# Kernel tuning notes

Measured on AMD Instinct MI355X. Metric: run time of the kernel, lower is better.

The kernel has to match this reference:

```python
import jax, jax.numpy as jnp
import numpy as np

EPS = 1e-8

def unit_projection(x):
    # project each embedding vector so its Fourier coefficients have unit magnitude
    f = jnp.fft.fft(x, axis=-1)
    f = f / jnp.maximum(jnp.abs(f), EPS)
    return jnp.real(jnp.fft.ifft(f, axis=-1))

def bind(a, b):
    return jnp.fft.irfft(jnp.fft.rfft(a, axis=-1) * jnp.fft.rfft(b, axis=-1), n=a.shape[-1], axis=-1)

def unbind(s, k):
    # k is unit-magnitude in Fourier domain, so its inverse is its conjugate
    return jnp.fft.irfft(jnp.fft.rfft(s, axis=-1) * jnp.conj(jnp.fft.rfft(k, axis=-1)), n=s.shape[-1], axis=-1)

def layer_norm(x, g, b):
    mu = jnp.mean(x, axis=-1, keepdims=True)
    var = jnp.var(x, axis=-1, keepdims=True)
    return (x - mu) * jax.lax.rsqrt(var + 1e-5) * g + b

def setup_inputs():
    key = jax.random.key(0)
    ks = jax.random.split(key, 12)
    B, S, D = 4, 2048, 1024
    sc = 1.0 / np.sqrt(D)
    inp = {
        'x': jax.random.normal(ks[0], (B, S, D), jnp.float32),
        'Wq': jax.random.normal(ks[1], (D, D), jnp.float32) * sc,
        'bq': jnp.zeros((D,), jnp.float32),
        'Wk': jax.random.normal(ks[2], (D, D), jnp.float32) * sc,
        'bk': jnp.zeros((D,), jnp.float32),
        'Wv': jax.random.normal(ks[3], (D, D), jnp.float32) * sc,
        'bv': jnp.zeros((D,), jnp.float32),
        'ln1_g': jnp.ones((D,), jnp.float32), 'ln1_b': jnp.zeros((D,), jnp.float32),
        'ln2_g': jnp.ones((D,), jnp.float32), 'ln2_b': jnp.zeros((D,), jnp.float32),
        'W1': jax.random.normal(ks[4], (D, 4 * D), jnp.float32) * sc,
        'b1': jnp.zeros((4 * D,), jnp.float32),
        'W2': jax.random.normal(ks[5], (4 * D, D), jnp.float32) * (1.0 / np.sqrt(4 * D)),
        'b2': jnp.zeros((D,), jnp.float32),
    }
    return inp

def reference(x, Wq, bq, Wk, bk, Wv, bv, ln1_g, ln1_b, ln2_g, ln2_b, W1, b1, W2, b2):
    h = layer_norm(x, ln1_g, ln1_b)
    q = unit_projection(h @ Wq + bq)
    k = unit_projection(h @ Wk + bk)
    v = unit_projection(h @ Wv + bv)
    s = jnp.cumsum(bind(k, v), axis=1)  # causal prefix-sum over sequence
    mixed = unbind(s, q)
    x = x + mixed  # dropout=0.0
    h2 = layer_norm(x, ln2_g, ln2_b)
    mlp = jax.nn.gelu(h2 @ W1 + b1, approximate=False) @ W2 + b2
    return x + mlp
```

## Files before the change

### kernel.cpp

```cpp
#include <hip/hip_runtime.h>
#include <cstdint>
#include <cstddef>

#define DD 1024
#define SSEQ 2048
#define NB 4
#define MROWS 8192
#define FBINS 513
#define FPAD 520
#define WFP 1152
#define NQKV 3456
#define NHID 4096
#define NCHUNK 64
#define SCHUNK 32

typedef _Float16 f16_t;
typedef _Float16 f16x8 __attribute__((ext_vector_type(8)));
typedef _Float16 f16x2 __attribute__((ext_vector_type(2)));
typedef float f32x4 __attribute__((ext_vector_type(4)));

__device__ __forceinline__ float2 cmul(float2 a, float2 b) {
  return make_float2(a.x * b.x - a.y * b.y, a.x * b.y + a.y * b.x);
}

__device__ __forceinline__ void async_cp16(const void* g, void* l) {
  __builtin_amdgcn_global_load_lds(
      (const __attribute__((address_space(1))) void*)g,
      (__attribute__((address_space(3))) void*)l, 16, 0, 0);
}

template <int N> __device__ __forceinline__ void vwait();
template <> __device__ __forceinline__ void vwait<0>() { asm volatile("s_waitcnt vmcnt(0)" ::: "memory"); }
template <> __device__ __forceinline__ void vwait<1>() { asm volatile("s_waitcnt vmcnt(1)" ::: "memory"); }
template <> __device__ __forceinline__ void vwait<2>() { asm volatile("s_waitcnt vmcnt(2)" ::: "memory"); }
template <> __device__ __forceinline__ void vwait<3>() { asm volatile("s_waitcnt vmcnt(3)" ::: "memory"); }
template <> __device__ __forceinline__ void vwait<4>() { asm volatile("s_waitcnt vmcnt(4)" ::: "memory"); }

__device__ __forceinline__ float fast_gelu(float val) {
  float av = __builtin_fabsf(val);
  float z = av * 0.70710678118654752f;
  float t = __builtin_amdgcn_rcpf(__builtin_fmaf(0.3275911f, z, 1.0f));
  float poly = t * __builtin_fmaf(t,
      __builtin_fmaf(t, __builtin_fmaf(t,
          __builtin_fmaf(t, 1.061405429f, -1.453152027f),
          1.421413741f), -0.284496736f), 0.254829592f);
  float e = __builtin_amdgcn_exp2f(z * z * -1.4426950408889634f);
  float w = poly * e;
  float r = fmaxf(val, 0.0f);
  return __builtin_fmaf(-0.5f * av, w, r);
}

__device__ __forceinline__ void fft1024(float2* bufA, float2* bufB,
                                        const float2* tw, int tid) {
  float2* s = bufA;
  float2* d = bufB;
  for (int m = 1; m < 1024; m <<= 1) {
#pragma unroll
    for (int r2 = 0; r2 < 2; ++r2) {
      int u = tid + r2 * 256;
      int k = u & (m - 1);
      int jm = u - k;
      float2 c0 = s[u];
      float2 c1 = s[u + 512];
      float2 wt = tw[jm];
      float2 su = make_float2(c0.x + c1.x, c0.y + c1.y);
      float2 df = make_float2(c0.x - c1.x, c0.y - c1.y);
      float2 pr = cmul(wt, df);
      d[2 * jm + k] = su;
      d[2 * jm + k + m] = pr;
    }
    __syncthreads();
    float2* tmp = s; s = d; d = tmp;
  }
}

__device__ __forceinline__ float2* fft512(float2* bufA, float2* bufB,
                                          const float2* tw, int tid) {
  float2* s = bufA;
  float2* d = bufB;
  for (int m = 1; m < 512; m <<= 1) {
    int u = tid;
    int k = u & (m - 1);
    int jm = u - k;
    float2 c0 = s[u];
    float2 c1 = s[u + 256];
    float2 wt = tw[jm];
    float2 su = make_float2(c0.x + c1.x, c0.y + c1.y);
    float2 df = make_float2(c0.x - c1.x, c0.y - c1.y);
    float2 pr = cmul(wt, df);
    d[2 * jm + k] = su;
    d[2 * jm + k + m] = pr;
    __syncthreads();
    float2* tmp = s; s = d; d = tmp;
  }
  return s;
}

__global__ __launch_bounds__(256) void wfft_k(
    const float* __restrict__ Wq, const float* __restrict__ Wk,
    const float* __restrict__ Wv, float* __restrict__ WfAll) {
  __shared__ float2 tw[512];
  __shared__ float2 bufA[1024];
  __shared__ float2 bufB[1024];
  const int tid = threadIdx.x;
  const int p = blockIdx.x >> 10, k = blockIdx.x & 1023;
  const float* W = (p == 0) ? Wq : ((p == 1) ? Wk : Wv);
  for (int t = tid; t < 512; t += 256) {
    float ang = -6.2831853071795864769f * (float)t * (1.0f / 1024.0f);
    tw[t] = make_float2(cosf(ang), sinf(ang));
  }
  const float* src = W + (size_t)k * DD;
  for (int t = tid; t < 1024; t += 256) bufA[t] = make_float2(src[t], 0.f);
  __syncthreads();
  fft1024(bufA, bufB, tw, tid);
  float* dst = WfAll + ((size_t)p * DD + k) * WFP;
  for (int t = tid; t <= 512; t += 256) {
    float2 f = bufA[t];
    dst[2 * t] = f.x;
    dst[2 * t + 1] = f.y;
  }
  for (int j = 1026 + tid; j < WFP; j += 256) dst[j] = 0.f;
}

__global__ __launch_bounds__(256) void bfft_k(
    const float* __restrict__ bq, const float* __restrict__ bk,
    const float* __restrict__ bv, float* __restrict__ biasC) {
  __shared__ float2 tw[512];
  __shared__ float2 bufA[1024];
  __shared__ float2 bufB[1024];
  const int tid = threadIdx.x;
  const int p = blockIdx.x;
  const float* bsrc = (p == 0) ? bq : ((p == 1) ? bk : bv);
  for (int t = tid; t < 512; t += 256) {
    float ang = -6.2831853071795864769f * (float)t * (1.0f / 1024.0f);
    tw[t] = make_float2(cosf(ang), sinf(ang));
  }
  for (int t = tid; t < 1024; t += 256) bufA[t] = make_float2(bsrc[t], 0.f);
  __syncthreads();
  fft1024(bufA, bufB, tw, tid);
  float* dst = biasC + (size_t)p * WFP;
  for (int t = tid; t <= 512; t += 256) {
    float2 f = bufA[t];
    dst[2 * t] = f.x;
    dst[2 * t + 1] = f.y;
  }
  for (int j = 1026 + tid; j < WFP; j += 256) dst[j] = 0.f;
}

__global__ __launch_bounds__(256) void transpose_cast_k(
    const float* __restrict__ W, f16_t* __restrict__ Wt, int K, int N) {
  __shared__ float tile[32][33];
  const int tx = threadIdx.x & 31, ty = threadIdx.x >> 5;
  const int n0 = blockIdx.x * 32, k0 = blockIdx.y * 32;
#pragma unroll
  for (int i = 0; i < 32; i += 8)
    tile[ty + i][tx] = W[(size_t)(k0 + ty + i) * N + n0 + tx];
  __syncthreads();
#pragma unroll
  for (int i = 0; i < 32; i += 8)
    Wt[(size_t)(n0 + ty + i) * K + k0 + tx] = (f16_t)tile[tx][ty + i];
}

__global__ __launch_bounds__(256) void transpose_cast2_k(
    const float* __restrict__ W, f16_t* __restrict__ WtH,
    f16_t* __restrict__ WtL, int K, int N) {
  __shared__ float tile[32][33];
  const int tx = threadIdx.x & 31, ty = threadIdx.x >> 5;
  const int n0 = blockIdx.x * 32, k0 = blockIdx.y * 32;
#pragma unroll
  for (int i = 0; i < 32; i += 8)
    tile[ty + i][tx] = W[(size_t)(k0 + ty + i) * N + n0 + tx];
  __syncthreads();
#pragma unroll
  for (int i = 0; i < 32; i += 8) {
    float val = tile[tx][ty + i];
    f16_t hi = (f16_t)val;
    f16_t lo = (f16_t)(val - (float)hi);
    size_t idx = (size_t)(n0 + ty + i) * K + k0 + tx;
    WtH[idx] = hi;
    WtL[idx] = lo;
  }
}

__global__ __launch_bounds__(256) void ln_cast2_k(
    const float* __restrict__ x, const float* __restrict__ g,
    const float* __restrict__ b, f16_t* __restrict__ hH,
    f16_t* __restrict__ hL) {
  const int row = blockIdx.x, tid = threadIdx.x;
  __shared__ float red[8];
  const float* xr = x + (size_t)row * DD;
  float v[4], ls = 0.f, lq = 0.f;
#pragma unroll
  for (int i = 0; i < 4; ++i) {
    v[i] = xr[i * 256 + tid];
    ls += v[i];
    lq += v[i] * v[i];
  }
#pragma unroll
  for (int o = 32; o > 0; o >>= 1) {
    ls += __shfl_down(ls, o);
    lq += __shfl_down(lq, o);
  }
  const int lane = tid & 63, w = tid >> 6;
  if (lane == 0) { red[w] = ls; red[w + 4] = lq; }
  __syncthreads();
  const float S = red[0] + red[1] + red[2] + red[3];
  const float Q = red[4] + red[5] + red[6] + red[7];
  const float mean = S * (1.f / 1024.f);
  const float var = Q * (1.f / 1024.f) - mean * mean;
  const float rs = rsqrtf(var + 1e-5f);
#pragma unroll
  for (int i = 0; i < 4; ++i) {
    int n = i * 256 + tid;
    float val = (v[i] - mean) * rs * g[n] + b[n];
    f16_t hi = (f16_t)val;
    hH[(size_t)row * DD + n] = hi;
    hL[(size_t)row * DD + n] = (f16_t)(val - (float)hi);
  }
}

__global__ __launch_bounds__(256, 2) void gemm_qkv_k(
    const f16_t* __restrict__ Ahi, const f16_t* __restrict__ Alo,
    const f16_t* __restrict__ Bhi, const float* __restrict__ bias,
    float* __restrict__ outF) {
  __shared__ alignas(16) f16_t AsH[128 * 64];
  __shared__ alignas(16) f16_t AsL[128 * 64];
  __shared__ alignas(16) f16_t BsH[128 * 64];
  const int tid = threadIdx.x;
  const int lane = tid & 63;
  const int w = tid >> 6;
  const int wm = w >> 1, wn = w & 1;

  const int lin = blockIdx.x;
  const int s = (lin & 7) * 216 + (lin >> 3);
  const int g = s / 108;
  const int r = s % 108;
  const int n = r >> 2;
  const int m0 = g * 4 + (r & 3);
  const int bn = n * 128;
  const int bm = m0 * 128;
  const bool qmode = (n < 9);

  f32x4 acc[4][4];
#pragma unroll
  for (int i = 0; i < 4; ++i)
#pragma unroll
    for (int j = 0; j < 4; ++j) acc[i][j] = (f32x4){0.f, 0.f, 0.f, 0.f};

  const int srow = lane >> 3;
  const int slot = lane & 7;

  for (int kt = 0; kt < 1024; kt += 64) {
#pragma unroll
    for (int i = 0; i < 4; ++i) {
      const int rb = (i * 4 + w) * 8;
      const int row = rb + srow;
      const int gg = (slot - (row & 7)) & 7;
      size_t ga = (size_t)(bm + row) * 1024 + kt + gg * 8;
      size_t gb = (size_t)(bn + row) * 1024 + kt + gg * 8;
      async_cp16(Ahi + ga, &AsH[rb * 64]);
      if (qmode) async_cp16(Alo + ga, &AsL[rb * 64]);
      async_cp16(Bhi + gb, &BsH[rb * 64]);
    }
    __syncthreads();
#pragma unroll
    for (int ks = 0; ks < 2; ++ks) {
      const int cgbase = ks * 4 + (lane >> 4);
      f16x8 ah[4], bh[4];
#pragma unroll
      for (int mt = 0; mt < 4; ++mt) {
        int m = wm * 64 + mt * 16 + (lane & 15);
        int sl = (cgbase + (m & 7)) & 7;
        ah[mt] = *(const f16x8*)(&AsH[m * 64 + sl * 8]);
      }
#pragma unroll
      for (int nt = 0; nt < 4; ++nt) {
        int nn = wn * 64 + nt * 16 + (lane & 15);
        int sl = (cgbase + (nn & 7)) & 7;
        bh[nt] = *(const f16x8*)(&BsH[nn * 64 + sl * 8]);
      }
#pragma unroll
      for (int mt = 0; mt < 4; ++mt)
#pragma unroll
        for (int nt = 0; nt < 4; ++nt)
          acc[mt][nt] = __builtin_amdgcn_mfma_f32_16x16x32_f16(
              ah[mt], bh[nt], acc[mt][nt], 0, 0, 0);
      if (qmode) {
        f16x8 al[4];
#pragma unroll
        for (int mt = 0; mt < 4; ++mt) {
          int m = wm * 64 + mt * 16 + (lane & 15);
          int sl = (cgbase + (m & 7)) & 7;
          al[mt] = *(const f16x8*)(&AsL[m * 64 + sl * 8]);
        }
#pragma unroll
        for (int mt = 0; mt < 4; ++mt)
#pragma unroll
          for (int nt = 0; nt < 4; ++nt)
            acc[mt][nt] = __builtin_amdgcn_mfma_f32_16x16x32_f16(
                al[mt], bh[nt], acc[mt][nt], 0, 0, 0);
      }
    }
    __syncthreads();
  }

  const int q = lane >> 4;
  const int cn = lane & 15;
#pragma unroll
  for (int mt = 0; mt < 4; ++mt) {
#pragma unroll
    for (int nt = 0; nt < 4; ++nt) {
      const int gcol = bn + wn * 64 + nt * 16 + cn;
      const float bv = bias[gcol];
      const int grow0 = bm + wm * 64 + mt * 16 + q * 4;
#pragma unroll
      for (int i = 0; i < 4; ++i) {
        size_t idx = (size_t)(grow0 + i) * NQKV + gcol;
        outF[idx] = acc[mt][nt][i] + bv;
      }
    }
  }
}

template <int RHALF>
__device__ __forceinline__ void stage_half(const f16_t* __restrict__ G,
                                           int grow0, int ldk, int kt,
                                           f16_t* ls, int w, int lane) {
  const int srow = lane >> 3;
  const int slot = lane & 7;
#pragma unroll
  for (int j = 0; j < RHALF / 64; ++j) {
    const int rb = (w + j * 8) * 8;
    const int row = rb + srow;
    const int gg = (slot - (row & 7)) & 7;
    async_cp16(G + (size_t)(grow0 + row) * ldk + kt + gg * 8, ls + rb * 64);
  }
}

template <int BM, int BN>
__device__ __forceinline__ void readA(const f16_t* As, int mq, int wm, int lane,
                                      f16x8 (&aR)[BM / 64][2]) {
#pragma unroll
  for (int mf = 0; mf < BM / 64; ++mf) {
    const int m = mq * (BM / 2) + wm * (BM / 4) + mf * 16 + (lane & 15);
#pragma unroll
    for (int ks = 0; ks < 2; ++ks) {
      const int cg = ks * 4 + (lane >> 4);
      const int sl = (cg + (m & 7)) & 7;
      aR[mf][ks] = *(const f16x8*)(As + m * 64 + sl * 8);
    }
  }
}

template <int BM, int BN>
__device__ __forceinline__ void readB(const f16_t* Bs, int nq, int wn, int lane,
                                      f16x8 (&bR)[BN / 128][2]) {
#pragma unroll
  for (int nf = 0; nf < BN / 128; ++nf) {
    const int n = nq * (BN / 2) + wn * (BN / 8) + nf * 16 + (lane & 15);
#pragma unroll
    for (int ks = 0; ks < 2; ++ks) {
      const int cg = ks * 4 + (lane >> 4);
      const int sl = (cg + (n & 7)) & 7;
      bR[nf][ks] = *(const f16x8*)(Bs + n * 64 + sl * 8);
    }
  }
}

template <int MF, int NF>
__device__ __forceinline__ void mfma_q(f32x4 (&acc)[MF][NF],
                                       const f16x8 (&aR)[MF][2],
                                       const f16x8 (&bR)[NF][2]) {
#pragma unroll
  for (int ks = 0; ks < 2; ++ks)
#pragma unroll
    for (int mf = 0; mf < MF; ++mf)
#pragma unroll
      for (int nf = 0; nf < NF; ++nf)
        acc[mf][nf] = __builtin_amdgcn_mfma_f32_16x16x32_f16(
            aR[mf][ks], bR[nf][ks], acc[mf][nf], 0, 0, 0);
}

template <int BM, int BN, int MM, int NN, int KK, int EPI>
__global__ __launch_bounds__(512, 2) void gemm8p_k(
    const f16_t* __restrict__ A, const f16_t* __restrict__ Bt,
    const float* __restrict__ bias, const float* __restrict__ resid,
    float* __restrict__ outF, f16_t* __restrict__ outH) {
  constexpr int MF = BM / 64;
  constexpr int NF = BN / 128;
  constexpr int LA = BM / 128;
  constexpr int LB = BN / 128;
  constexpr int NT = KK / 64;
  constexpr int TILE = (BM + BN) * 64;
  __shared__ alignas(16) f16_t lds[2 * TILE];

  const int tid = threadIdx.x;
  const int lane = tid & 63;
  const int w = tid >> 6;
  const int wm = w >> 2;
  const int wn = w & 3;

  constexpr int ntm = MM / BM, ntn = NN / BN;
  constexpr int per = (ntm * ntn) / 8;
  const int lin = (int)blockIdx.x;
  const int s = (lin & 7) * per + (lin >> 3);
  const int bn = (s % ntn) * BN;
  const int bm = (s / ntn) * BM;

  f32x4 acc[2][2][MF][NF];
#pragma unroll
  for (int a0 = 0; a0 < 2; ++a0)
#pragma unroll
    for (int a1 = 0; a1 < 2; ++a1)
#pragma unroll
      for (int mf = 0; mf < MF; ++mf)
#pragma unroll
        for (int nf = 0; nf < NF; ++nf)
          acc[a0][a1][mf][nf] = (f32x4){0.f, 0.f, 0.f, 0.f};

  {
    f16_t* A0s = lds;
    f16_t* B0s = lds + BM * 64;
    stage_half<BM / 2>(A, bm, KK, 0, A0s, w, lane);
    stage_half<BN / 2>(Bt, bn, KK, 0, B0s, w, lane);
    stage_half<BN / 2>(Bt, bn + BN / 2, KK, 0, B0s + (BN / 2) * 64, w, lane);
    stage_half<BM / 2>(A, bm + BM / 2, KK, 0, A0s + (BM / 2) * 64, w, lane);
  }
  vwait<LA + LB>();
  __builtin_amdgcn_s_barrier();

  f16x8 aR[MF][2], bR0[NF][2], bR1[NF][2];

  for (int t = 0; t < NT; ++t) {
    const int cur = t & 1;
    f16_t* As = lds + cur * TILE;
    f16_t* Bs = As + BM * 64;
    f16_t* Asn = lds + (cur ^ 1) * TILE;
    f16_t* Bsn = Asn + BM * 64;
    const bool pre = (t + 1 < NT);
    const int ktn = (t + 1) << 6;

    readA<BM, BN>(As, 0, wm, lane, aR);
    readB<BM, BN>(Bs, 0, wn, lane, bR0);
    if (pre) stage_half<BM / 2>(A, bm, KK, ktn, Asn, w, lane);
    __builtin_amdgcn_s_barrier();
    __builtin_amdgcn_s_setprio(1);
    mfma_q<MF, NF>(acc[0][0], aR, bR0);
    __builtin_amdgcn_s_setprio(0);
    if (pre) vwait<2 * LA>(); else vwait<LA>();
    __builtin_amdgcn_s_barrier();

    readB<BM, BN>(Bs, 1, wn, lane, bR1);
    if (pre) stage_half<BN / 2>(Bt, bn, KK, ktn, Bsn, w, lane);
    __builtin_amdgcn_s_barrier();
    __builtin_amdgcn_s_setprio(1);
    mfma_q<MF, NF>(acc[0][1], aR, bR1);
    __builtin_amdgcn_s_setprio(0);
    if (pre) vwait<LA + LB>(); else vwait<0>();
    __builtin_amdgcn_s_barrier();

    readA<BM, BN>(As, 1, wm, lane, aR);
    if (pre) stage_half<BN / 2>(Bt, bn + BN / 2, KK, ktn,
                                Bsn + (BN / 2) * 64, w, lane);
    __builtin_amdgcn_s_barrier();
    __builtin_amdgcn_s_setprio(1);
    mfma_q<MF, NF>(acc[1][0], aR, bR0);
    __builtin_amdgcn_s_setprio(0);
    __builtin_amdgcn_s_barrier();

    if (pre) stage_half<BM / 2>(A, bm + BM / 2, KK, ktn,
                                Asn + (BM / 2) * 64, w, lane);
    __builtin_amdgcn_s_barrier();
    __builtin_amdgcn_s_setprio(1);
    mfma_q<MF, NF>(acc[1][1], aR, bR1);
    __builtin_amdgcn_s_setprio(0);
    if (pre) vwait<LA + LB>();
    __builtin_amdgcn_s_barrier();
  }

  const int q4 = lane >> 4;
  const int cn = lane & 15;
#pragma unroll
  for (int mq = 0; mq < 2; ++mq)
#pragma unroll
    for (int nq = 0; nq < 2; ++nq)
#pragma unroll
      for (int mf = 0; mf < MF; ++mf)
#pragma unroll
        for (int nf = 0; nf < NF; ++nf) {
          const int gcol = bn + nq * (BN / 2) + wn * (BN / 8) + nf * 16 + cn;
          const float bv = bias[gcol];
          const int grow0 = bm + mq * (BM / 2) + wm * (BM / 4) + mf * 16 + q4 * 4;
#pragma unroll
          for (int i = 0; i < 4; ++i) {
            const float val = acc[mq][nq][mf][nf][i] + bv;
            const size_t idx = (size_t)(grow0 + i) * NN + gcol;
            if (EPI == 1) {
              outH[idx] = (f16_t)fast_gelu(val);
            } else {
              outF[idx] = val + resid[idx];
            }
          }
        }
}

__device__ __forceinline__ float2 unitc(float2 a) {
  float inv = 1.0f / fmaxf(sqrtf(a.x * a.x + a.y * a.y), 1e-8f);
  return make_float2(a.x * inv, a.y * inv);
}
__device__ __forceinline__ float2 bind_bin(const float2* r, int f) {
  float2 kn = unitc(r[576 + f]);
  float2 vn = unitc(r[1152 + f]);
  return cmul(kn, vn);
}

__global__ __launch_bounds__(256) void scan_pass1_k(
    const float* __restrict__ qkvF, float2* __restrict__ T) {
  const int bid = blockIdx.x;
  const int sc = bid & 63;
  const int fh = (bid >> 6) & 1;
  const int b = bid >> 7;
  const int s0 = sc * SCHUNK;
  const float2* base = (const float2*)(qkvF + ((size_t)(b * SSEQ + s0)) * NQKV);
  for (int f = fh * 256 + threadIdx.x; f < FBINS; f += 512) {
    float2 acc = make_float2(0.f, 0.f);
    const float2* r = base;
    for (int i = 0; i < SCHUNK; ++i) {
      float2 pv = bind_bin(r, f);
      acc.x += pv.x; acc.y += pv.y;
      r += NQKV / 2;
    }
    T[((size_t)b * NCHUNK + sc) * FBINS + f] = acc;
  }
}

__global__ void scan_pass2_k(float2* __restrict__ T) {
  const int idx = blockIdx.x * 256 + threadIdx.x;
  if (idx >= NB * FBINS) return;
  const int b = idx / FBINS, f = idx % FBINS;
  float2 acc = make_float2(0.f, 0.f);
  for (int sc = 0; sc < NCHUNK; ++sc) {
    size_t a = ((size_t)b * NCHUNK + sc) * FBINS + f;
    float2 v = T[a];
    T[a] = acc;
    acc.x += v.x; acc.y += v.y;
  }
}

__global__ __launch_bounds__(256) void scan_pass3_k(
    const float* __restrict__ qkvF, const float2* __restrict__ T,
    float2* __restrict__ Scum) {
  const int bid = blockIdx.x;
  const int sc = bid & 63;
  const int fh = (bid >> 6) & 1;
  const int b = bid >> 7;
  const int s0 = sc * SCHUNK;
  const float2* base = (const float2*)(qkvF + ((size_t)(b * SSEQ + s0)) * NQKV);
  for (int f = fh * 256 + threadIdx.x; f < FBINS; f += 512) {
    float2 acc = T[((size_t)b * NCHUNK + sc) * FBINS + f];
    const float2* r = base;
    size_t orow = ((size_t)(b * SSEQ + s0)) * FPAD + f;
    for (int i = 0; i < SCHUNK; ++i) {
      float2 pv = bind_bin(r, f);
      acc.x += pv.x; acc.y += pv.y;
      Scum[orow] = acc;
      r += NQKV / 2;
      orow += FPAD;
    }
  }
}

__global__ __launch_bounds__(256) void unbind_ln2_k(
    const float2* __restrict__ Scum, const float* __restrict__ qkvF,
    const float* __restrict__ x, float* __restrict__ x2out,
    f16_t* __restrict__ h2, const float* __restrict__ g2,
    const float* __restrict__ b2) {
  __shared__ float2 tw[256];
  __shared__ float2 Marr[513];
  __shared__ float2 bufA[512];
  __shared__ float2 bufB[512];
  __shared__ float red[8];
  const int tid = threadIdx.x;
  const int row = blockIdx.x;

  {
    float ang = 6.2831853071795864769f * (float)tid * (1.0f / 512.0f);
    tw[tid] = make_float2(cosf(ang), sinf(ang));
  }
  const float2* qrow = (const float2*)(qkvF + (size_t)row * NQKV);
  for (int t = tid; t <= 512; t += 256) {
    float2 sc = Scum[(size_t)row * FPAD + t];
    float2 fq = unitc(qrow[t]);
    Marr[t] = make_float2(sc.x * fq.x + sc.y * fq.y, sc.y * fq.x - sc.x * fq.y);
  }
  __syncthreads();
#pragma unroll
  for (int rr = 0; rr < 2; ++rr) {
    int t = tid + rr * 256;
    float2 a = Marr[t];
    float2 b = Marr[512 - t];
    float2 E = make_float2(0.5f * (a.x + b.x), 0.5f * (a.y - b.y));
    float2 Dd = make_float2(0.5f * (a.x - b.x), 0.5f * (a.y + b.y));
    float ang = 6.2831853071795864769f * (float)t * (1.0f / 1024.0f);
    float cw = cosf(ang), sw = sinf(ang);
    float2 O = make_float2(cw * Dd.x - sw * Dd.y, cw * Dd.y + sw * Dd.x);
    bufA[t] = make_float2(E.x - O.y, E.y + O.x);
  }
  __syncthreads();
  float2* res = fft512(bufA, bufB, tw, tid);

  const float* xr = x + (size_t)row * DD;
  float v[2][2];
  float ls = 0.f, lq = 0.f;
#pragma unroll
  for (int rr = 0; rr < 2; ++rr) {
    int n = tid + rr * 256;
    float2 z = res[n];
    float2 xv = *(const float2*)(xr + 2 * n);
    float v0 = xv.x + z.x * (1.0f / 512.0f);
    float v1 = xv.y + z.y * (1.0f / 512.0f);
    *(float2*)(x2out + (size_t)row * DD + 2 * n) = make_float2(v0, v1);
    v[rr][0] = v0; v[rr][1] = v1;
    ls += v0 + v1;
    lq += v0 * v0 + v1 * v1;
  }
#pragma unroll
  for (int o = 32; o > 0; o >>= 1) {
    ls += __shfl_down(ls, o);
    lq += __shfl_down(lq, o);
  }
  const int lane = tid & 63, w = tid >> 6;
  if (lane == 0) { red[w] = ls; red[w + 4] = lq; }
  __syncthreads();
  const float S = red[0] + red[1] + red[2] + red[3];
  const float Q = red[4] + red[5] + red[6] + red[7];
  const float mean = S * (1.f / 1024.f);
  const float var = Q * (1.f / 1024.f) - mean * mean;
  const float rs = rsqrtf(var + 1e-5f);
  f16_t* hr = h2 + (size_t)row * DD;
#pragma unroll
  for (int rr = 0; rr < 2; ++rr) {
    int n = tid + rr * 256;
    float2 gv = *(const float2*)(g2 + 2 * n);
    float2 bv = *(const float2*)(b2 + 2 * n);
    f16x2 hp;
    hp[0] = (f16_t)((v[rr][0] - mean) * rs * gv.x + bv.x);
    hp[1] = (f16_t)((v[rr][1] - mean) * rs * gv.y + bv.y);
    *(f16x2*)(hr + 2 * n) = hp;
  }
}

extern "C" void kernel_launch(void* const* d_in, const int* in_sizes, int n_in,
                              void* d_out, int out_size, void* d_ws,
                              size_t ws_size, hipStream_t stream) {
  const float* x     = (const float*)d_in[0];
  const float* Wq    = (const float*)d_in[1];
  const float* bq    = (const float*)d_in[2];
  const float* Wk    = (const float*)d_in[3];
  const float* bk    = (const float*)d_in[4];
  const float* Wv    = (const float*)d_in[5];
  const float* bv    = (const float*)d_in[6];
  const float* ln1_g = (const float*)d_in[7];
  const float* ln1_b = (const float*)d_in[8];
  const float* ln2_g = (const float*)d_in[9];
  const float* ln2_b = (const float*)d_in[10];
  const float* W1    = (const float*)d_in[11];
  const float* b1    = (const float*)d_in[12];
  const float* W2    = (const float*)d_in[13];
  const float* b2    = (const float*)d_in[14];
  float* out = (float*)d_out;

  char* p = (char*)d_ws;
  auto take = [&](size_t bytes) {
    char* r = p;
    p += (bytes + 255) & ~(size_t)255;
    return r;
  };
  f16_t* BtH   = (f16_t*)take((size_t)NQKV * DD * sizeof(f16_t));
  f16_t* BtL   = (f16_t*)take((size_t)NQKV * DD * sizeof(f16_t));
  f16_t* W1T   = (f16_t*)take((size_t)NHID * DD * sizeof(f16_t));
  f16_t* W2T   = (f16_t*)take((size_t)DD * NHID * sizeof(f16_t));
  float* biasC = (float*)take((size_t)NQKV * sizeof(float));
  f16_t* hbuf  = (f16_t*)take((size_t)MROWS * DD * sizeof(f16_t));
  char*  big   = take((size_t)MROWS * NQKV * sizeof(float));
  float2* Scum = (float2*)take((size_t)MROWS * FPAD * sizeof(float2));
  float* x2    = (float*)take((size_t)MROWS * DD * sizeof(float));
  float2* Tch  = (float2*)take((size_t)NB * NCHUNK * FBINS * sizeof(float2));
  float* WfAll   = (float*)big;
  float* qkv_f   = (float*)big;
  f16_t* mlp1    = (f16_t*)big;
  f16_t* hlo     = (f16_t*)x2;

  wfft_k<<<3 * DD, 256, 0, stream>>>(Wq, Wk, Wv, WfAll);
  for (int pp = 0; pp < 3; ++pp)
    transpose_cast2_k<<<dim3(WFP / 32, DD / 32), 256, 0, stream>>>(
        WfAll + (size_t)pp * DD * WFP,
        BtH + (size_t)pp * WFP * DD,
        BtL + (size_t)pp * WFP * DD, DD, WFP);
  bfft_k<<<3, 256, 0, stream>>>(bq, bk, bv, biasC);
  transpose_cast_k<<<dim3(128, 32), 256, 0, stream>>>(W1, W1T, DD, NHID);
  transpose_cast_k<<<dim3(32, 128), 256, 0, stream>>>(W2, W2T, NHID, DD);

  ln_cast2_k<<<MROWS, 256, 0, stream>>>(x, ln1_g, ln1_b, hbuf, hlo);

  gemm_qkv_k<<<(NQKV / 128) * (MROWS / 128), 256, 0, stream>>>(
      hbuf, hlo, BtH, biasC, qkv_f);

  scan_pass1_k<<<NB * NCHUNK * 2, 256, 0, stream>>>(qkv_f, Tch);
  scan_pass2_k<<<(NB * FBINS + 255) / 256, 256, 0, stream>>>(Tch);
  scan_pass3_k<<<NB * NCHUNK * 2, 256, 0, stream>>>(qkv_f, Tch, Scum);

  unbind_ln2_k<<<MROWS, 256, 0, stream>>>(Scum, qkv_f, x, x2, hbuf, ln2_g, ln2_b);

  gemm8p_k<256, 256, MROWS, NHID, DD, 1><<<512, 512, 0, stream>>>(
      hbuf, W1T, b1, nullptr, nullptr, mlp1);

  gemm8p_k<128, 256, MROWS, DD, NHID, 2><<<256, 512, 0, stream>>>(
      mlp1, W2T, b2, x2, out, nullptr);
}
```

Measured before the change: 497.0 us.

## Replace QKV GEMM with 256x128 double-buffered 8-wave pipelined kernel

Swaps the simple single-buffered 128x128 QKV GEMM for a 512-thread, 256x128-tile kernel that double-buffers LDS, interleaves async staging with MFMA quarters, and raises wave priority around the MFMA sections. The q-columns' hi/lo split of A is folded into a 32-step K loop that streams Ahi and then Alo, replacing the separate inner lo pass. The unused BtL buffer and its two-output transpose are dropped in favour of the plain cast transpose. The aim is better latency hiding and higher MFMA utilisation, at the cost of a more complex schedule and a hand-balanced block-to-XCD mapping.

```diff
diff --git a/kernel.cpp b/kernel.cpp
--- a/kernel.cpp
+++ b/kernel.cpp
@@ -161,27 +161,6 @@
     Wt[(size_t)(n0 + ty + i) * K + k0 + tx] = (f16_t)tile[tx][ty + i];
 }
 
-__global__ __launch_bounds__(256) void transpose_cast2_k(
-    const float* __restrict__ W, f16_t* __restrict__ WtH,
-    f16_t* __restrict__ WtL, int K, int N) {
-  __shared__ float tile[32][33];
-  const int tx = threadIdx.x & 31, ty = threadIdx.x >> 5;
-  const int n0 = blockIdx.x * 32, k0 = blockIdx.y * 32;
-#pragma unroll
-  for (int i = 0; i < 32; i += 8)
-    tile[ty + i][tx] = W[(size_t)(k0 + ty + i) * N + n0 + tx];
-  __syncthreads();
-#pragma unroll
-  for (int i = 0; i < 32; i += 8) {
-    float val = tile[tx][ty + i];
-    f16_t hi = (f16_t)val;
-    f16_t lo = (f16_t)(val - (float)hi);
-    size_t idx = (size_t)(n0 + ty + i) * K + k0 + tx;
-    WtH[idx] = hi;
-    WtL[idx] = lo;
-  }
-}
-
 __global__ __launch_bounds__(256) void ln_cast2_k(
     const float* __restrict__ x, const float* __restrict__ g,
     const float* __restrict__ b, f16_t* __restrict__ hH,
@@ -216,109 +195,6 @@
     f16_t hi = (f16_t)val;
     hH[(size_t)row * DD + n] = hi;
     hL[(size_t)row * DD + n] = (f16_t)(val - (float)hi);
-  }
-}
-
-__global__ __launch_bounds__(256, 2) void gemm_qkv_k(
-    const f16_t* __restrict__ Ahi, const f16_t* __restrict__ Alo,
-    const f16_t* __restrict__ Bhi, const float* __restrict__ bias,
-    float* __restrict__ outF) {
-  __shared__ alignas(16) f16_t AsH[128 * 64];
-  __shared__ alignas(16) f16_t AsL[128 * 64];
-  __shared__ alignas(16) f16_t BsH[128 * 64];
-  const int tid = threadIdx.x;
-  const int lane = tid & 63;
-  const int w = tid >> 6;
-  const int wm = w >> 1, wn = w & 1;
-
-  const int lin = blockIdx.x;
-  const int s = (lin & 7) * 216 + (lin >> 3);
-  const int g = s / 108;
-  const int r = s % 108;
-  const int n = r >> 2;
-  const int m0 = g * 4 + (r & 3);
-  const int bn = n * 128;
-  const int bm = m0 * 128;
-  const bool qmode = (n < 9);
-
-  f32x4 acc[4][4];
-#pragma unroll
-  for (int i = 0; i < 4; ++i)
-#pragma unroll
-    for (int j = 0; j < 4; ++j) acc[i][j] = (f32x4){0.f, 0.f, 0.f, 0.f};
-
-  const int srow = lane >> 3;
-  const int slot = lane & 7;
-
-  for (int kt = 0; kt < 1024; kt += 64) {
-#pragma unroll
-    for (int i = 0; i < 4; ++i) {
-      const int rb = (i * 4 + w) * 8;
-      const int row = rb + srow;
-      const int gg = (slot - (row & 7)) & 7;
-      size_t ga = (size_t)(bm + row) * 1024 + kt + gg * 8;
-      size_t gb = (size_t)(bn + row) * 1024 + kt + gg * 8;
-      async_cp16(Ahi + ga, &AsH[rb * 64]);
-      if (qmode) async_cp16(Alo + ga, &AsL[rb * 64]);
-      async_cp16(Bhi + gb, &BsH[rb * 64]);
-    }
-    __syncthreads();
-#pragma unroll
-    for (int ks = 0; ks < 2; ++ks) {
-      const int cgbase = ks * 4 + (lane >> 4);
-      f16x8 ah[4], bh[4];
-#pragma unroll
-      for (int mt = 0; mt < 4; ++mt) {
-        int m = wm * 64 + mt * 16 + (lane & 15);
-        int sl = (cgbase + (m & 7)) & 7;
-        ah[mt] = *(const f16x8*)(&AsH[m * 64 + sl * 8]);
-      }
-#pragma unroll
-      for (int nt = 0; nt < 4; ++nt) {
-        int nn = wn * 64 + nt * 16 + (lane & 15);
-        int sl = (cgbase + (nn & 7)) & 7;
-        bh[nt] = *(const f16x8*)(&BsH[nn * 64 + sl * 8]);
-      }
-#pragma unroll
-      for (int mt = 0; mt < 4; ++mt)
-#pragma unroll
-        for (int nt = 0; nt < 4; ++nt)
-          acc[mt][nt] = __builtin_amdgcn_mfma_f32_16x16x32_f16(
-              ah[mt], bh[nt], acc[mt][nt], 0, 0, 0);
-      if (qmode) {
-        f16x8 al[4];
-#pragma unroll
-        for (int mt = 0; mt < 4; ++mt) {
-          int m = wm * 64 + mt * 16 + (lane & 15);
-          int sl = (cgbase + (m & 7)) & 7;
-          al[mt] = *(const f16x8*)(&AsL[m * 64 + sl * 8]);
-        }
-#pragma unroll
-        for (int mt = 0; mt < 4; ++mt)
-#pragma unroll
-          for (int nt = 0; nt < 4; ++nt)
-            acc[mt][nt] = __builtin_amdgcn_mfma_f32_16x16x32_f16(
-                al[mt], bh[nt], acc[mt][nt], 0, 0, 0);
-      }
-    }
-    __syncthreads();
-  }
-
-  const int q = lane >> 4;
-  const int cn = lane & 15;
-#pragma unroll
-  for (int mt = 0; mt < 4; ++mt) {
-#pragma unroll
-    for (int nt = 0; nt < 4; ++nt) {
-      const int gcol = bn + wn * 64 + nt * 16 + cn;
-      const float bv = bias[gcol];
-      const int grow0 = bm + wm * 64 + mt * 16 + q * 4;
-#pragma unroll
-      for (int i = 0; i < 4; ++i) {
-        size_t idx = (size_t)(grow0 + i) * NQKV + gcol;
-        outF[idx] = acc[mt][nt][i] + bv;
-      }
-    }
   }
 }
 
@@ -500,6 +376,132 @@
             } else {
               outF[idx] = val + resid[idx];
             }
+          }
+        }
+}
+
+__global__ __launch_bounds__(512, 2) void gemm_qkv8p_k(
+    const f16_t* __restrict__ Ahi, const f16_t* __restrict__ Alo,
+    const f16_t* __restrict__ Bt, const float* __restrict__ bias,
+    float* __restrict__ outF) {
+  constexpr int BM = 256, BN = 128;
+  constexpr int MF = 4, NF = 1;
+  constexpr int LA = 2, LB = 1;
+  constexpr int TILE = (BM + BN) * 64;
+  __shared__ alignas(16) f16_t lds[2 * TILE];
+
+  const int tid = threadIdx.x;
+  const int lane = tid & 63;
+  const int w = tid >> 6;
+  const int wm = w >> 2, wn = w & 3;
+
+  const int lin = (int)blockIdx.x;
+  const int xcd = lin & 7, idx = lin >> 3;
+  int bm, bn;
+  bool qmode;
+  if (idx < 36) {
+    const int h = xcd * 36 + idx;
+    bm = (h / 9) * 256;
+    bn = (h % 9) * 128;
+    qmode = true;
+  } else {
+    const int l = xcd * 72 + (idx - 36);
+    bm = (l / 18) * 256;
+    bn = 1152 + (l % 18) * 128;
+    qmode = false;
+  }
+  const int NT = qmode ? 32 : 16;
+
+  f32x4 acc[2][2][MF][NF];
+#pragma unroll
+  for (int a0 = 0; a0 < 2; ++a0)
+#pragma unroll
+    for (int a1 = 0; a1 < 2; ++a1)
+#pragma unroll
+      for (int mf = 0; mf < MF; ++mf)
+#pragma unroll
+        for (int nf = 0; nf < NF; ++nf)
+          acc[a0][a1][mf][nf] = (f32x4){0.f, 0.f, 0.f, 0.f};
+
+  {
+    f16_t* A0s = lds;
+    f16_t* B0s = lds + BM * 64;
+    stage_half<BM / 2>(Ahi, bm, DD, 0, A0s, w, lane);
+    stage_half<BN / 2>(Bt, bn, DD, 0, B0s, w, lane);
+    stage_half<BN / 2>(Bt, bn + BN / 2, DD, 0, B0s + (BN / 2) * 64, w, lane);
+    stage_half<BM / 2>(Ahi, bm + BM / 2, DD, 0, A0s + (BM / 2) * 64, w, lane);
+  }
+  vwait<LA + LB>();
+  __builtin_amdgcn_s_barrier();
+
+  f16x8 aR[MF][2], bR0[NF][2], bR1[NF][2];
+
+  for (int t = 0; t < NT; ++t) {
+    const int cur = t & 1;
+    f16_t* As = lds + cur * TILE;
+    f16_t* Bs = As + BM * 64;
+    f16_t* Asn = lds + (cur ^ 1) * TILE;
+    f16_t* Bsn = Asn + BM * 64;
+    const bool pre = (t + 1 < NT);
+    const int tt = t + 1;
+    const f16_t* An = (qmode && tt >= 16) ? Alo : Ahi;
+    const int ktn = (tt & 15) << 6;
+
+    readA<BM, BN>(As, 0, wm, lane, aR);
+    readB<BM, BN>(Bs, 0, wn, lane, bR0);
+    if (pre) stage_half<BM / 2>(An, bm, DD, ktn, Asn, w, lane);
+    __builtin_amdgcn_s_barrier();
+    __builtin_amdgcn_s_setprio(1);
+    mfma_q<MF, NF>(acc[0][0], aR, bR0);
+    __builtin_amdgcn_s_setprio(0);
+    if (pre) vwait<2 * LA>(); else vwait<LA>();
+    __builtin_amdgcn_s_barrier();
+
+    readB<BM, BN>(Bs, 1, wn, lane, bR1);
+    if (pre) stage_half<BN / 2>(Bt, bn, DD, ktn, Bsn, w, lane);
+    __builtin_amdgcn_s_barrier();
+    __builtin_amdgcn_s_setprio(1);
+    mfma_q<MF, NF>(acc[0][1], aR, bR1);
+    __builtin_amdgcn_s_setprio(0);
+    if (pre) vwait<LA + LB>(); else vwait<0>();
+    __builtin_amdgcn_s_barrier();
+
+    readA<BM, BN>(As, 1, wm, lane, aR);
+    if (pre) stage_half<BN / 2>(Bt, bn + BN / 2, DD, ktn,
+                                Bsn + (BN / 2) * 64, w, lane);
+    __builtin_amdgcn_s_barrier();
+    __builtin_amdgcn_s_setprio(1);
+    mfma_q<MF, NF>(acc[1][0], aR, bR0);
+    __builtin_amdgcn_s_setprio(0);
+    __builtin_amdgcn_s_barrier();
+
+    if (pre) stage_half<BM / 2>(An, bm + BM / 2, DD, ktn,
+                                Asn + (BM / 2) * 64, w, lane);
+    __builtin_amdgcn_s_barrier();
+    __builtin_amdgcn_s_setprio(1);
+    mfma_q<MF, NF>(acc[1][1], aR, bR1);
+    __builtin_amdgcn_s_setprio(0);
+    if (pre) vwait<LA + LB>();
+    __builtin_amdgcn_s_barrier();
+  }
+
+  const int q4 = lane >> 4;
+  const int cn = lane & 15;
+#pragma unroll
+  for (int mq = 0; mq < 2; ++mq)
+#pragma unroll
+    for (int nq = 0; nq < 2; ++nq)
+#pragma unroll
+      for (int mf = 0; mf < MF; ++mf)
+#pragma unroll
+        for (int nf = 0; nf < NF; ++nf) {
+          const int gcol = bn + nq * (BN / 2) + wn * (BN / 8) + nf * 16 + cn;
+          const float bv = bias[gcol];
+          const int grow0 = bm + mq * (BM / 2) + wm * (BM / 4) + mf * 16 + q4 * 4;
+#pragma unroll
+          for (int i = 0; i < 4; ++i) {
+            const size_t oidx = (size_t)(grow0 + i) * NQKV + gcol;
+            outF[oidx] = acc[mq][nq][mf][nf][i] + bv;
           }
         }
 }
@@ -677,7 +679,6 @@
     return r;
   };
   f16_t* BtH   = (f16_t*)take((size_t)NQKV * DD * sizeof(f16_t));
-  f16_t* BtL   = (f16_t*)take((size_t)NQKV * DD * sizeof(f16_t));
   f16_t* W1T   = (f16_t*)take((size_t)NHID * DD * sizeof(f16_t));
   f16_t* W2T   = (f16_t*)take((size_t)DD * NHID * sizeof(f16_t));
   float* biasC = (float*)take((size_t)NQKV * sizeof(float));
@@ -693,18 +694,16 @@
 
   wfft_k<<<3 * DD, 256, 0, stream>>>(Wq, Wk, Wv, WfAll);
   for (int pp = 0; pp < 3; ++pp)
-    transpose_cast2_k<<<dim3(WFP / 32, DD / 32), 256, 0, stream>>>(
+    transpose_cast_k<<<dim3(WFP / 32, DD / 32), 256, 0, stream>>>(
         WfAll + (size_t)pp * DD * WFP,
-        BtH + (size_t)pp * WFP * DD,
-        BtL + (size_t)pp * WFP * DD, DD, WFP);
+        BtH + (size_t)pp * WFP * DD, DD, WFP);
   bfft_k<<<3, 256, 0, stream>>>(bq, bk, bv, biasC);
   transpose_cast_k<<<dim3(128, 32), 256, 0, stream>>>(W1, W1T, DD, NHID);
   transpose_cast_k<<<dim3(32, 128), 256, 0, stream>>>(W2, W2T, NHID, DD);
 
   ln_cast2_k<<<MROWS, 256, 0, stream>>>(x, ln1_g, ln1_b, hbuf, hlo);
 
-  gemm_qkv_k<<<(NQKV / 128) * (MROWS / 128), 256, 0, stream>>>(
-      hbuf, hlo, BtH, biasC, qkv_f);
+  gemm_qkv8p_k<<<864, 512, 0, stream>>>(hbuf, hlo, BtH, biasC, qkv_f);
 
   scan_pass1_k<<<NB * NCHUNK * 2, 256, 0, stream>>>(qkv_f, Tch);
   scan_pass2_k<<<(NB * FBINS + 255) / 256, 256, 0, stream>>>(Tch);
```

Result: slower. 520.3 us (+4.7%).
